# Performance work log

Hardware: AMD Instinct MI355X
Metric: run time of the kernel (lower is better)

The kernel has to match this reference:

```python
import jax, jax.numpy as jnp
import numpy as np

OUT = 7          # output_size
SR = 2           # sampling_ratio
CANON_SIZE = 224.0
CANON_LVL = 4
MIN_LVL, MAX_LVL = 2, 5
SCALES = (0.25, 0.125, 0.0625, 0.03125)
IMG = 1024.0


def _roi_align(feat, batch_idx, boxes, scale):
    """ROIAlign aligned=True. feat [B,C,H,W], boxes [R,4] (x1,y1,x2,y2) in image coords.
    Returns [R,C,OUT,OUT]."""
    B, C, H, W = feat.shape
    R = boxes.shape[0]
    x1 = boxes[:, 0] * scale - 0.5
    y1 = boxes[:, 1] * scale - 0.5
    x2 = boxes[:, 2] * scale - 0.5
    y2 = boxes[:, 3] * scale - 0.5
    bin_w = (x2 - x1) / OUT
    bin_h = (y2 - y1) / OUT
    S = OUT * SR
    # sample positions in bin units: bin p, sub-sample i -> p + (i+0.5)/SR
    g = (jnp.arange(S, dtype=feat.dtype) + 0.5) / SR
    ys = y1[:, None] + g[None, :] * bin_h[:, None]   # [R,S]
    xs = x1[:, None] + g[None, :] * bin_w[:, None]   # [R,S]
    vy = (ys >= -1.0) & (ys <= H)
    vx = (xs >= -1.0) & (xs <= W)
    yc = jnp.clip(ys, 0.0, H - 1)
    xc = jnp.clip(xs, 0.0, W - 1)
    y0 = jnp.floor(yc).astype(jnp.int32)
    x0 = jnp.floor(xc).astype(jnp.int32)
    y1i = jnp.minimum(y0 + 1, H - 1)
    x1i = jnp.minimum(x0 + 1, W - 1)
    ly = yc - y0.astype(feat.dtype); hy = 1.0 - ly
    lx = xc - x0.astype(feat.dtype); hx = 1.0 - lx
    f = jnp.transpose(feat, (0, 2, 3, 1))            # [B,H,W,C]
    b = batch_idx[:, None, None]                     # [R,1,1]

    def gather(yi, xi):
        # advanced indexing broadcast -> [R,S,S,C]
        return f[b, yi[:, :, None], xi[:, None, :], :]

    def w2(wy, wx):
        return (wy[:, :, None] * wx[:, None, :])[..., None]

    v = (gather(y0, x0) * w2(hy, hx)
         + gather(y0, x1i) * w2(hy, lx)
         + gather(y1i, x0) * w2(ly, hx)
         + gather(y1i, x1i) * w2(ly, lx))             # [R,S,S,C]
    mask = (vy[:, :, None] & vx[:, None, :])[..., None]
    v = jnp.where(mask, v, jnp.zeros((), feat.dtype))
    v = v.reshape(R, OUT, SR, OUT, SR, C).mean(axis=(2, 4))  # avg over SRxSR samples
    return jnp.transpose(v, (0, 3, 1, 2))            # [R,C,OUT,OUT]


def setup_inputs() -> dict:
    key = jax.random.key(0)
    k2, k3, k4, k5, kwh, kc = jax.random.split(key, 6)
    B, C, N = 2, 256, 256
    x2 = jax.random.normal(k2, (B, C, 256, 256), jnp.float32)
    x3 = jax.random.normal(k3, (B, C, 128, 128), jnp.float32)
    x4 = jax.random.normal(k4, (B, C, 64, 64), jnp.float32)
    x5 = jax.random.normal(k5, (B, C, 32, 32), jnp.float32)
    wh = jax.random.uniform(kwh, (B, N, 2), jnp.float32, 32.0, 480.0)
    cxy = jax.random.uniform(kc, (B, N, 2), jnp.float32, 0.0, IMG)
    p1 = jnp.clip(cxy - wh / 2, 0.0, IMG)
    p2 = jnp.clip(cxy + wh / 2, 0.0, IMG)
    boxes = jnp.concatenate([p1, p2], axis=-1)  # [B,N,4] = (x1,y1,x2,y2)
    return {"x2": x2, "x3": x3, "x4": x4, "x5": x5, "boxes": boxes}


def reference(x2, x3, x4, x5, boxes):
    B, N, _ = boxes.shape
    flat = boxes.reshape(B * N, 4)
    batch_idx = jnp.repeat(jnp.arange(B, dtype=jnp.int32), N)
    # FPN level assignment
    area = (flat[:, 2] - flat[:, 0]) * (flat[:, 3] - flat[:, 1])
    sizes = jnp.sqrt(area)
    lvl = jnp.floor(CANON_LVL + jnp.log2(sizes / CANON_SIZE + 1e-8))
    lvl = jnp.clip(lvl, MIN_LVL, MAX_LVL).astype(jnp.int32) - MIN_LVL  # [R] in {0..3}
    feats = (x2, x3, x4, x5)
    C = x2.shape[1]
    out = jnp.zeros((B * N, C, OUT, OUT), x2.dtype)
    for l, (f, s) in enumerate(zip(feats, SCALES)):
        pooled = _roi_align(f, batch_idx, flat, s)
        out = jnp.where((lvl == l)[:, None, None, None], pooled, out)
    return out
```

## Files before the change

### kernel.cpp

```cpp
#include <hip/hip_runtime.h>


#define OUTD 7
#define SRD  2
#define SD   14
#define CCH  256
#define NBOX 256
#define NC   8
#define NCHK (CCH / NC)
#define CAPP 513
#define NBIN (OUTD * OUTD)

__global__ __launch_bounds__(256) void roi_direct(
    const float* __restrict__ f0, const float* __restrict__ f1,
    const float* __restrict__ f2, const float* __restrict__ f3,
    const float* __restrict__ boxes, float* __restrict__ out)
{
    const int roi = blockIdx.x;
    const int c0  = blockIdx.y * NC;
    const int t   = threadIdx.x;
    const int b   = roi / NBOX;

    const float bx1 = boxes[roi * 4 + 0];
    const float by1 = boxes[roi * 4 + 1];
    const float bx2 = boxes[roi * 4 + 2];
    const float by2 = boxes[roi * 4 + 3];

    const float area = (bx2 - bx1) * (by2 - by1);
    const float sz   = sqrtf(area);
    int lvl = (int)floorf(4.0f + log2f(sz * (1.0f / 224.0f) + 1e-8f));
    lvl = min(max(lvl, 2), 5) - 2;

    const int   H     = 256 >> lvl;
    const int   W     = H;
    const float scale = 1.0f / (float)(4 << lvl);
    const size_t HW   = (size_t)H * (size_t)W;

    const float* f  = (lvl == 0) ? f0 : (lvl == 1) ? f1 : (lvl == 2) ? f2 : f3;
    const float* fb = f + (size_t)b * CCH * HW;

    __shared__ int   s_ax0[SD], s_ax1[SD], s_ay0[SD], s_ay1[SD];
    __shared__ float s_wxh[SD], s_wxl[SD], s_wyh[SD], s_wyl[SD];
    __shared__ float s_win[NC * CAPP];
    __shared__ float s_out[NC * NBIN];

    if (t < SD) {
        const int i = t;
        const float x1r = bx1 * scale - 0.5f;
        const float y1r = by1 * scale - 0.5f;
        const float x2r = bx2 * scale - 0.5f;
        const float y2r = by2 * scale - 0.5f;
        const float bw = (x2r - x1r) * (1.0f / OUTD);
        const float bh = (y2r - y1r) * (1.0f / OUTD);
        const float g  = ((float)i + 0.5f) * (1.0f / SRD);
        const float ys = y1r + g * bh;
        const float xs = x1r + g * bw;
        const float vy = ((ys >= -1.0f) && (ys <= (float)H)) ? 1.0f : 0.0f;
        const float vx = ((xs >= -1.0f) && (xs <= (float)W)) ? 1.0f : 0.0f;
        const float yc = fminf(fmaxf(ys, 0.0f), (float)(H - 1));
        const float xc = fminf(fmaxf(xs, 0.0f), (float)(W - 1));
        const int y0 = (int)yc;
        const int x0 = (int)xc;
        const float ly = yc - (float)y0;
        const float lx = xc - (float)x0;
        s_ay0[i] = y0;
        s_ay1[i] = min(y0 + 1, H - 1);
        s_ax0[i] = x0;
        s_ax1[i] = min(x0 + 1, W - 1);
        s_wyh[i] = vy * (1.0f - ly);
        s_wyl[i] = vy * ly;
        s_wxh[i] = vx * (1.0f - lx);
        s_wxl[i] = vx * lx;
    }
    __syncthreads();

    int x_lo = s_ax0[0], x_hi = s_ax1[0], y_lo = s_ay0[0], y_hi = s_ay1[0];
    #pragma unroll
    for (int j = 1; j < SD; ++j) {
        x_lo = min(x_lo, s_ax0[j]); x_hi = max(x_hi, s_ax1[j]);
        y_lo = min(y_lo, s_ay0[j]); y_hi = max(y_hi, s_ay1[j]);
    }
    const int Ww = x_hi - x_lo + 1;
    const int Hw = y_hi - y_lo + 1;

    const int c_idx = t / 49;
    const int bin   = t - c_idx * 49;
    const int oy    = bin / 7;
    const int ox    = bin - oy * 7;
    const int ia = 2 * oy, ib = ia + 1;
    const int ja = 2 * ox, jb = ja + 1;

    if (Hw * Ww <= CAPP) {
        const int hw   = t >> 5;
        const int l32  = t & 31;
        const int nruns = NC * Hw;
        for (int run = hw; run < nruns; run += 8) {
            const int c = run & (NC - 1);
            const int y = run >> 3;
            const float* src = fb + (size_t)(c0 + c) * HW
                                  + (size_t)(y_lo + y) * W + x_lo;
            float* dst = s_win + c * CAPP + y * Ww;
            for (int x = l32; x < Ww; x += 32)
                dst[x] = src[x];
        }
        __syncthreads();

        if (t < 245) {
            const int ryA0 = (s_ay0[ia] - y_lo) * Ww, ryA1 = (s_ay1[ia] - y_lo) * Ww;
            const int ryB0 = (s_ay0[ib] - y_lo) * Ww, ryB1 = (s_ay1[ib] - y_lo) * Ww;
            const int rxA0 = s_ax0[ja] - x_lo,        rxA1 = s_ax1[ja] - x_lo;
            const int rxB0 = s_ax0[jb] - x_lo,        rxB1 = s_ax1[jb] - x_lo;
            const float wyAh = s_wyh[ia], wyAl = s_wyl[ia];
            const float wyBh = s_wyh[ib], wyBl = s_wyl[ib];
            const float wxAh = s_wxh[ja], wxAl = s_wxl[ja];
            const float wxBh = s_wxh[jb], wxBl = s_wxl[jb];
            for (int ci = c_idx; ci < NC; ci += 5) {
                const float* w = s_win + ci * CAPP;
                const float acc =
                    wyAh * (wxAh * w[ryA0 + rxA0] + wxAl * w[ryA0 + rxA1])
                  + wyAl * (wxAh * w[ryA1 + rxA0] + wxAl * w[ryA1 + rxA1])
                  + wyAh * (wxBh * w[ryA0 + rxB0] + wxBl * w[ryA0 + rxB1])
                  + wyAl * (wxBh * w[ryA1 + rxB0] + wxBl * w[ryA1 + rxB1])
                  + wyBh * (wxAh * w[ryB0 + rxA0] + wxAl * w[ryB0 + rxA1])
                  + wyBl * (wxAh * w[ryB1 + rxA0] + wxAl * w[ryB1 + rxA1])
                  + wyBh * (wxBh * w[ryB0 + rxB0] + wxBl * w[ryB0 + rxB1])
                  + wyBl * (wxBh * w[ryB1 + rxB0] + wxBl * w[ryB1 + rxB1]);
                s_out[ci * NBIN + bin] = acc * 0.25f;
            }
        }
        __syncthreads();

        float* ob = out + (size_t)roi * (CCH * NBIN) + (size_t)c0 * NBIN;
        for (int i = t; i < NC * NBIN; i += 256)
            ob[i] = s_out[i];
    } else {
        const int yA0g = s_ay0[ia] * W, yA1g = s_ay1[ia] * W;
        const int yB0g = s_ay0[ib] * W, yB1g = s_ay1[ib] * W;
        const int xA0 = s_ax0[ja], xA1 = s_ax1[ja];
        const int xB0 = s_ax0[jb], xB1 = s_ax1[jb];
        const float wyAh = s_wyh[ia], wyAl = s_wyl[ia];
        const float wyBh = s_wyh[ib], wyBl = s_wyl[ib];
        const float wxAh = s_wxh[ja], wxAl = s_wxl[ja];
        const float wxBh = s_wxh[jb], wxBl = s_wxl[jb];
        float* ob = out + (size_t)roi * (CCH * NBIN) + (size_t)c0 * NBIN;
        for (int idx = t; idx < NC * NBIN; idx += 256) {
            const int ci = idx / NBIN;
            const int bn = idx - ci * NBIN;
            const int oy2 = bn / 7, ox2 = bn - (bn / 7) * 7;
            const int i2a = 2 * oy2, i2b = i2a + 1;
            const int j2a = 2 * ox2, j2b = j2a + 1;
            const float* fc = fb + (size_t)(c0 + ci) * HW;
            const float acc =
                s_wyh[i2a] * (s_wxh[j2a] * fc[s_ay0[i2a] * W + s_ax0[j2a]] + s_wxl[j2a] * fc[s_ay0[i2a] * W + s_ax1[j2a]])
              + s_wyl[i2a] * (s_wxh[j2a] * fc[s_ay1[i2a] * W + s_ax0[j2a]] + s_wxl[j2a] * fc[s_ay1[i2a] * W + s_ax1[j2a]])
              + s_wyh[i2a] * (s_wxh[j2b] * fc[s_ay0[i2a] * W + s_ax0[j2b]] + s_wxl[j2b] * fc[s_ay0[i2a] * W + s_ax1[j2b]])
              + s_wyl[i2a] * (s_wxh[j2b] * fc[s_ay1[i2a] * W + s_ax0[j2b]] + s_wxl[j2b] * fc[s_ay1[i2a] * W + s_ax1[j2b]])
              + s_wyh[i2b] * (s_wxh[j2a] * fc[s_ay0[i2b] * W + s_ax0[j2a]] + s_wxl[j2a] * fc[s_ay0[i2b] * W + s_ax1[j2a]])
              + s_wyl[i2b] * (s_wxh[j2a] * fc[s_ay1[i2b] * W + s_ax0[j2a]] + s_wxl[j2a] * fc[s_ay1[i2b] * W + s_ax1[j2a]])
              + s_wyh[i2b] * (s_wxh[j2b] * fc[s_ay0[i2b] * W + s_ax0[j2b]] + s_wxl[j2b] * fc[s_ay0[i2b] * W + s_ax1[j2b]])
              + s_wyl[i2b] * (s_wxh[j2b] * fc[s_ay1[i2b] * W + s_ax0[j2b]] + s_wxl[j2b] * fc[s_ay1[i2b] * W + s_ax1[j2b]]);
            ob[idx] = acc * 0.25f;
        }
        (void)yA0g; (void)yA1g; (void)yB0g; (void)yB1g;
        (void)xA0; (void)xA1; (void)xB0; (void)xB1;
        (void)wyAh; (void)wyAl; (void)wyBh; (void)wyBl;
        (void)wxAh; (void)wxAl; (void)wxBh; (void)wxBl;
    }
}

extern "C" void kernel_launch(void* const* d_in, const int* in_sizes, int n_in,
                              void* d_out, int out_size, void* d_ws, size_t ws_size,
                              hipStream_t stream) {
    const float* f0    = (const float*)d_in[0];
    const float* f1    = (const float*)d_in[1];
    const float* f2    = (const float*)d_in[2];
    const float* f3    = (const float*)d_in[3];
    const float* boxes = (const float*)d_in[4];
    float*       outp  = (float*)d_out;

    const int R = out_size / (CCH * NBIN);
    roi_direct<<<dim3(R, NCHK), 256, 0, stream>>>(f0, f1, f2, f3, boxes, outp);
}
```

Baseline: 305.4 us.

## Stage ROI window via direct global-to-LDS loads with 4 channels per block

Replaces the register-staged row copy into shared memory with the global_load_lds builtin, which writes the ROI window into LDS directly using flattened offsets. It cuts channels per block from 8 to 4 and enlarges the per-channel window so more boxes take the LDS path instead of the gather fallback. It also drops the shared output staging buffer, so each thread writes its result straight to global memory. The trade-off is twice as many blocks, a float-division index decode per element, and per-element rather than row-coalesced loads.

```diff
diff --git a/kernel.cpp b/kernel.cpp
--- a/kernel.cpp
+++ b/kernel.cpp
@@ -6,10 +6,18 @@
 #define SD   14
 #define CCH  256
 #define NBOX 256
-#define NC   8
+#define NC   4
 #define NCHK (CCH / NC)
-#define CAPP 513
+#define CAPP 1091
+#define LMAX (CAPP - 63)
 #define NBIN (OUTD * OUTD)
+
+typedef __attribute__((address_space(1))) unsigned int gu32;
+typedef __attribute__((address_space(3))) unsigned int lu32;
+
+__device__ __forceinline__ void gl2lds(const float* g, float* l) {
+    __builtin_amdgcn_global_load_lds((gu32*)(unsigned long long)g, (lu32*)l, 4, 0, 0);
+}
 
 __global__ __launch_bounds__(256) void roi_direct(
     const float* __restrict__ f0, const float* __restrict__ f1,
@@ -31,10 +39,11 @@
     int lvl = (int)floorf(4.0f + log2f(sz * (1.0f / 224.0f) + 1e-8f));
     lvl = min(max(lvl, 2), 5) - 2;
 
-    const int   H     = 256 >> lvl;
+    const int   wsh   = 8 - lvl;
+    const int   H     = 1 << wsh;
     const int   W     = H;
     const float scale = 1.0f / (float)(4 << lvl);
-    const size_t HW   = (size_t)H * (size_t)W;
+    const size_t HW   = (size_t)1 << (2 * wsh);
 
     const float* f  = (lvl == 0) ? f0 : (lvl == 1) ? f1 : (lvl == 2) ? f2 : f3;
     const float* fb = f + (size_t)b * CCH * HW;
@@ -42,7 +51,6 @@
     __shared__ int   s_ax0[SD], s_ax1[SD], s_ay0[SD], s_ay1[SD];
     __shared__ float s_wxh[SD], s_wxl[SD], s_wyh[SD], s_wyl[SD];
     __shared__ float s_win[NC * CAPP];
-    __shared__ float s_out[NC * NBIN];
 
     if (t < SD) {
         const int i = t;
@@ -82,30 +90,36 @@
     }
     const int Ww = x_hi - x_lo + 1;
     const int Hw = y_hi - y_lo + 1;
+    const int L  = Hw * Ww;
 
-    const int c_idx = t / 49;
-    const int bin   = t - c_idx * 49;
-    const int oy    = bin / 7;
-    const int ox    = bin - oy * 7;
+    const int ci  = t / NBIN;
+    const int bin = t - ci * NBIN;
+    const int oy  = bin / 7;
+    const int ox  = bin - oy * 7;
     const int ia = 2 * oy, ib = ia + 1;
     const int ja = 2 * ox, jb = ja + 1;
 
-    if (Hw * Ww <= CAPP) {
-        const int hw   = t >> 5;
-        const int l32  = t & 31;
-        const int nruns = NC * Hw;
-        for (int run = hw; run < nruns; run += 8) {
-            const int c = run & (NC - 1);
-            const int y = run >> 3;
-            const float* src = fb + (size_t)(c0 + c) * HW
-                                  + (size_t)(y_lo + y) * W + x_lo;
-            float* dst = s_win + c * CAPP + y * Ww;
-            for (int x = l32; x < Ww; x += 32)
-                dst[x] = src[x];
+    float* ob = out + (size_t)roi * (CCH * NBIN) + (size_t)c0 * NBIN;
+
+    if (L <= LMAX) {
+        const float inv = 1.0f / (float)Ww;
+        const int wv = t >> 6, ln = t & 63;
+        const int ub = (y_lo << wsh) + x_lo;
+        for (int c = 0; c < NC; ++c) {
+            const float* cb = fb + (size_t)(c0 + c) * HW + ub;
+            float* lb = s_win + c * CAPP;
+            for (int o0 = wv * 64; o0 < L; o0 += 256) {
+                int o = min(o0 + ln, L - 1);
+                int y = (int)((float)o * inv);
+                int x = o - y * Ww;
+                if (x < 0)   { x += Ww; --y; }
+                if (x >= Ww) { x -= Ww; ++y; }
+                gl2lds(cb + (y << wsh) + x, lb + o0);
+            }
         }
         __syncthreads();
 
-        if (t < 245) {
+        if (t < NC * NBIN) {
             const int ryA0 = (s_ay0[ia] - y_lo) * Ww, ryA1 = (s_ay1[ia] - y_lo) * Ww;
             const int ryB0 = (s_ay0[ib] - y_lo) * Ww, ryB1 = (s_ay1[ib] - y_lo) * Ww;
             const int rxA0 = s_ax0[ja] - x_lo,        rxA1 = s_ax1[ja] - x_lo;
@@ -114,57 +128,32 @@
             const float wyBh = s_wyh[ib], wyBl = s_wyl[ib];
             const float wxAh = s_wxh[ja], wxAl = s_wxl[ja];
             const float wxBh = s_wxh[jb], wxBl = s_wxl[jb];
-            for (int ci = c_idx; ci < NC; ci += 5) {
-                const float* w = s_win + ci * CAPP;
-                const float acc =
-                    wyAh * (wxAh * w[ryA0 + rxA0] + wxAl * w[ryA0 + rxA1])
-                  + wyAl * (wxAh * w[ryA1 + rxA0] + wxAl * w[ryA1 + rxA1])
-                  + wyAh * (wxBh * w[ryA0 + rxB0] + wxBl * w[ryA0 + rxB1])
-                  + wyAl * (wxBh * w[ryA1 + rxB0] + wxBl * w[ryA1 + rxB1])
-                  + wyBh * (wxAh * w[ryB0 + rxA0] + wxAl * w[ryB0 + rxA1])
-                  + wyBl * (wxAh * w[ryB1 + rxA0] + wxAl * w[ryB1 + rxA1])
-                  + wyBh * (wxBh * w[ryB0 + rxB0] + wxBl * w[ryB0 + rxB1])
-                  + wyBl * (wxBh * w[ryB1 + rxB0] + wxBl * w[ryB1 + rxB1]);
-                s_out[ci * NBIN + bin] = acc * 0.25f;
-            }
+            const float* w = s_win + ci * CAPP;
+            const float acc =
+                wyAh * (wxAh * w[ryA0 + rxA0] + wxAl * w[ryA0 + rxA1])
+              + wyAl * (wxAh * w[ryA1 + rxA0] + wxAl * w[ryA1 + rxA1])
+              + wyAh * (wxBh * w[ryA0 + rxB0] + wxBl * w[ryA0 + rxB1])
+              + wyAl * (wxBh * w[ryA1 + rxB0] + wxBl * w[ryA1 + rxB1])
+              + wyBh * (wxAh * w[ryB0 + rxA0] + wxAl * w[ryB0 + rxA1])
+              + wyBl * (wxAh * w[ryB1 + rxA0] + wxAl * w[ryB1 + rxA1])
+              + wyBh * (wxBh * w[ryB0 + rxB0] + wxBl * w[ryB0 + rxB1])
+              + wyBl * (wxBh * w[ryB1 + rxB0] + wxBl * w[ryB1 + rxB1]);
+            ob[t] = acc * 0.25f;
         }
-        __syncthreads();
-
-        float* ob = out + (size_t)roi * (CCH * NBIN) + (size_t)c0 * NBIN;
-        for (int i = t; i < NC * NBIN; i += 256)
-            ob[i] = s_out[i];
     } else {
-        const int yA0g = s_ay0[ia] * W, yA1g = s_ay1[ia] * W;
-        const int yB0g = s_ay0[ib] * W, yB1g = s_ay1[ib] * W;
-        const int xA0 = s_ax0[ja], xA1 = s_ax1[ja];
-        const int xB0 = s_ax0[jb], xB1 = s_ax1[jb];
-        const float wyAh = s_wyh[ia], wyAl = s_wyl[ia];
-        const float wyBh = s_wyh[ib], wyBl = s_wyl[ib];
-        const float wxAh = s_wxh[ja], wxAl = s_wxl[ja];
-        const float wxBh = s_wxh[jb], wxBl = s_wxl[jb];
-        float* ob = out + (size_t)roi * (CCH * NBIN) + (size_t)c0 * NBIN;
-        for (int idx = t; idx < NC * NBIN; idx += 256) {
-            const int ci = idx / NBIN;
-            const int bn = idx - ci * NBIN;
-            const int oy2 = bn / 7, ox2 = bn - (bn / 7) * 7;
-            const int i2a = 2 * oy2, i2b = i2a + 1;
-            const int j2a = 2 * ox2, j2b = j2a + 1;
+        if (t < NC * NBIN) {
             const float* fc = fb + (size_t)(c0 + ci) * HW;
             const float acc =
-                s_wyh[i2a] * (s_wxh[j2a] * fc[s_ay0[i2a] * W + s_ax0[j2a]] + s_wxl[j2a] * fc[s_ay0[i2a] * W + s_ax1[j2a]])
-              + s_wyl[i2a] * (s_wxh[j2a] * fc[s_ay1[i2a] * W + s_ax0[j2a]] + s_wxl[j2a] * fc[s_ay1[i2a] * W + s_ax1[j2a]])
-              + s_wyh[i2a] * (s_wxh[j2b] * fc[s_ay0[i2a] * W + s_ax0[j2b]] + s_wxl[j2b] * fc[s_ay0[i2a] * W + s_ax1[j2b]])
-              + s_wyl[i2a] * (s_wxh[j2b] * fc[s_ay1[i2a] * W + s_ax0[j2b]] + s_wxl[j2b] * fc[s_ay1[i2a] * W + s_ax1[j2b]])
-              + s_wyh[i2b] * (s_wxh[j2a] * fc[s_ay0[i2b] * W + s_ax0[j2a]] + s_wxl[j2a] * fc[s_ay0[i2b] * W + s_ax1[j2a]])
-              + s_wyl[i2b] * (s_wxh[j2a] * fc[s_ay1[i2b] * W + s_ax0[j2a]] + s_wxl[j2a] * fc[s_ay1[i2b] * W + s_ax1[j2a]])
-              + s_wyh[i2b] * (s_wxh[j2b] * fc[s_ay0[i2b] * W + s_ax0[j2b]] + s_wxl[j2b] * fc[s_ay0[i2b] * W + s_ax1[j2b]])
-              + s_wyl[i2b] * (s_wxh[j2b] * fc[s_ay1[i2b] * W + s_ax0[j2b]] + s_wxl[j2b] * fc[s_ay1[i2b] * W + s_ax1[j2b]]);
-            ob[idx] = acc * 0.25f;
+                s_wyh[ia] * (s_wxh[ja] * fc[s_ay0[ia] * W + s_ax0[ja]] + s_wxl[ja] * fc[s_ay0[ia] * W + s_ax1[ja]])
+              + s_wyl[ia] * (s_wxh[ja] * fc[s_ay1[ia] * W + s_ax0[ja]] + s_wxl[ja] * fc[s_ay1[ia] * W + s_ax1[ja]])
+              + s_wyh[ia] * (s_wxh[jb] * fc[s_ay0[ia] * W + s_ax0[jb]] + s_wxl[jb] * fc[s_ay0[ia] * W + s_ax1[jb]])
+              + s_wyl[ia] * (s_wxh[jb] * fc[s_ay1[ia] * W + s_ax0[jb]] + s_wxl[jb] * fc[s_ay1[ia] * W + s_ax1[jb]])
+              + s_wyh[ib] * (s_wxh[ja] * fc[s_ay0[ib] * W + s_ax0[ja]] + s_wxl[ja] * fc[s_ay0[ib] * W + s_ax1[ja]])
+              + s_wyl[ib] * (s_wxh[ja] * fc[s_ay1[ib] * W + s_ax0[ja]] + s_wxl[ja] * fc[s_ay1[ib] * W + s_ax1[ja]])
+              + s_wyh[ib] * (s_wxh[jb] * fc[s_ay0[ib] * W + s_ax0[jb]] + s_wxl[jb] * fc[s_ay0[ib] * W + s_ax1[jb]])
+              + s_wyl[ib] * (s_wxh[jb] * fc[s_ay1[ib] * W + s_ax0[jb]] + s_wxl[jb] * fc[s_ay1[ib] * W + s_ax1[jb]]);
+            ob[t] = acc * 0.25f;
         }
-        (void)yA0g; (void)yA1g; (void)yB0g; (void)yB1g;
-        (void)xA0; (void)xA1; (void)xB0; (void)xB1;
-        (void)wyAh; (void)wyAl; (void)wyBh; (void)wyBl;
-        (void)wxAh; (void)wxAl; (void)wxBh; (void)wxBl;
     }
 }
 
```

New measurement: 271.2 us. 1.13x faster.
